# Optimization experiments

Measured on AMD Instinct MI355X. Metric: run time of the kernel, lower is better.

The kernel has to match this reference:

```python
import jax, jax.numpy as jnp
import numpy as np

B, N, F, H, M, EF, OUT = 256, 32, 40, 100, 100, 4, 128
MESSAGE_PASSES = 3


def setup_inputs() -> dict:
    key = jax.random.key(0)
    ks = jax.random.split(key, 8)
    # Deterministic ring graphs: node i <-> node (i+1)%N, one-hot bond type.
    # Every node has degree 2 -> static nonzero counts.
    rng = np.random.default_rng(0)
    edges = np.zeros((B, N, N, EF), np.float32)
    b = np.arange(B)[:, None]
    i = np.arange(N)[None, :]
    j = (i + 1) % N
    t = rng.integers(0, EF, size=(B, N))
    edges[b, i, j, t] = 1.0
    edges[b, j, i, t] = 1.0

    nodes = jax.random.normal(ks[0], (B, N, F), jnp.float32)

    def init(k, shape, fan):
        return jax.random.normal(k, shape, jnp.float32) / np.sqrt(fan).astype(np.float32)

    W_msg = init(ks[1], (M, H, EF), H)          # MNN edge-conditioned weights
    W_ih = init(ks[2], (3 * H, M), M)            # GRUCell input weights
    W_hh = init(ks[3], (3 * H, H), H)            # GRUCell hidden weights
    b_ih = jnp.zeros((3 * H,), jnp.float32)
    b_hh = jnp.zeros((3 * H,), jnp.float32)
    Wg = init(ks[4], (H + F, H), H + F)          # gather gate
    bg = jnp.zeros((H,), jnp.float32)
    We = init(ks[5], (H, H), H)                  # gather embed
    be = jnp.zeros((H,), jnp.float32)
    Wo = init(ks[6], (H, OUT), H)                # output head
    bo = jnp.zeros((OUT,), jnp.float32)

    return {
        "nodes": nodes, "edges": jnp.asarray(edges),
        "W_msg": W_msg, "W_ih": W_ih, "W_hh": W_hh, "b_ih": b_ih, "b_hh": b_hh,
        "Wg": Wg, "bg": bg, "We": We, "be": be, "Wo": Wo, "bo": bo,
        "n_edges": B * N * 2, "n_node_entries": B * N,
    }


def gru_cell(x, h, W_ih, W_hh, b_ih, b_hh):
    gi = x @ W_ih.T + b_ih
    gh = h @ W_hh.T + b_hh
    ir, iz, inn = jnp.split(gi, 3, axis=-1)
    hr, hz, hn = jnp.split(gh, 3, axis=-1)
    r = jax.nn.sigmoid(ir + hr)
    z = jax.nn.sigmoid(iz + hz)
    n = jnp.tanh(inn + r * hn)
    return (1.0 - z) * n + z * h


def reference(nodes, edges, W_msg, W_ih, W_hh, b_ih, b_hh, Wg, bg, We, be, Wo, bo,
              n_edges, n_node_entries):
    adjacency = jnp.sum(edges, axis=3)                      # (B, N, N)
    eb, en, eg = jnp.nonzero(adjacency, size=n_edges)       # edge-level indices
    nb, nn_ = jnp.nonzero(adjacency.sum(-1), size=n_node_entries)

    # Dense one-hot segment-sum matrix: (n_node_entries, n_edges)
    same = (nb[:, None] == eb) & (nn_[:, None] == en)
    msg_sum_mat = same.astype(jnp.float32)

    edge_batch_edges = edges[eb, en, eg, :]                 # (E, EF)

    hidden = jnp.zeros((B, N, H), jnp.float32).at[:, :, :F].set(nodes)
    node_h = hidden[nb, nn_, :]                             # (V, H)

    for _ in range(MESSAGE_PASSES):
        nghb_h = hidden[eb, eg, :]                          # (E, H)
        # MNN message: sum_f edges[e,f] * W_msg[m,h,f] * nghb[e,h]
        message_terms = jnp.einsum('ef,mhf,eh->em', edge_batch_edges, W_msg, nghb_h)
        messages = msg_sum_mat @ message_terms              # (V, M) dense one-hot matmul
        node_h = gru_cell(messages, node_h, W_ih, W_hh, b_ih, b_hh)
        hidden = hidden.at[nb, nn_, :].set(node_h)

    node_mask = (adjacency.sum(-1) != 0).astype(jnp.float32)  # (B, N)
    cat = jnp.concatenate([hidden, nodes], axis=-1)           # (B, N, H+F)
    gate = jax.nn.sigmoid(cat @ Wg + bg)
    emb = gate * (hidden @ We + be)
    graph_emb = jnp.sum(emb * node_mask[..., None], axis=1)   # (B, H)
    return graph_emb @ Wo + bo                                # (B, OUT)
```

## Files before the change

### kernel.cpp

```cpp
#include <hip/hip_runtime.h>
#include <cstddef>
#include <cstdint>

#define B_   256
#define N_   32
#define F_   40
#define H_   100
#define OUT_ 128
#define TB   1024
#define XCS  168
#define XMS  136
#define ST2  40
#define NBLK 343
#define NLO  63

using bf16x8 = __attribute__((ext_vector_type(8))) short;
using f32x4  = __attribute__((ext_vector_type(4))) float;

#define MFMA(a,b,c) __builtin_amdgcn_mfma_f32_16x16x32_bf16((a),(b),(c),0,0,0)

__device__ __forceinline__ float sigmoidf_(float x){ return 1.0f/(1.0f+__expf(-x)); }
__device__ __forceinline__ float tanhf_(float x){
  float e = __expf(2.0f*x);
  return 1.0f - 2.0f/(e+1.0f);
}
__device__ __forceinline__ float bf2f(short s){ return __uint_as_float(((uint32_t)(uint16_t)s)<<16); }
__device__ __forceinline__ short f2bf(float x){
  uint32_t u = __float_as_uint(x);
  return (short)((u + 0x7FFFu + ((u>>16)&1u))>>16);
}
__device__ __forceinline__ void bsplit(float x, short& hi, short& lo){
  hi = f2bf(x);
  lo = f2bf(x - bf2f(hi));
}

__global__ void prep_frags4(const float* __restrict__ Wmsg,
                            const float* __restrict__ Wih,
                            const float* __restrict__ Whh,
                            const float* __restrict__ Wg,
                            const float* __restrict__ We,
                            short* __restrict__ AFhi,
                            short* __restrict__ AFlo){
  int slot = blockIdx.x*blockDim.x + threadIdx.x;
  if (slot >= NBLK*512) return;
  int blk = slot>>9, r = slot&511, lane = r>>3, jj = r&7;
  int m = lane&15, q = lane>>4, kl = q*8+jj;
  float v = 0.0f;
  if (blk < 112){
    int t = blk/28, rem = blk%28, jmt = rem>>2, ks = rem&3;
    int mg = jmt*16+m, h = ks*32+kl;
    if (mg<100 && h<100) v = Wmsg[(mg*100+h)*4 + t];
    AFhi[slot] = f2bf(v);
  } else if (blk < 280){
    int bb = blk-112, mat = bb/28, rem = bb%28, jmt = rem>>2, ks = rem&3;
    int mg = jmt*16+m, k = ks*32+kl;
    if (mg<100 && k<100)
      v = (mat<3) ? Wih[(mat*100+mg)*100+k] : Whh[((mat-3)*100+mg)*100+k];
    AFhi[slot] = f2bf(v);
  } else if (blk < 315){
    int bb = blk-280, jmt = bb/5, ks = bb%5;
    int mg = jmt*16+m, k = ks*32+kl;
    if (mg<100 && k<140) v = Wg[k*100+mg];
    short hi,lo; bsplit(v,hi,lo);
    AFhi[slot] = hi;
    AFlo[(size_t)(blk-280)*512 + r] = lo;
  } else {
    int bb = blk-315, jmt = bb>>2, ks = bb&3;
    int mg = jmt*16+m, k = ks*32+kl;
    if (mg<100 && k<100) v = We[k*100+mg];
    short hi,lo; bsplit(v,hi,lo);
    AFhi[slot] = hi;
    AFlo[(size_t)(blk-280)*512 + r] = lo;
  }
}

__global__ __launch_bounds__(TB, 4) void mpnn_mfma(
    const float* __restrict__ nodes, const float* __restrict__ edges,
    const short* __restrict__ AFhi, const short* __restrict__ AFlo,
    const float* __restrict__ b_ih, const float* __restrict__ b_hh,
    const float* __restrict__ bg, const float* __restrict__ be,
    const float* __restrict__ Wo, const float* __restrict__ bo,
    float* __restrict__ out){
  const int b = blockIdx.x;
  const int tid = threadIdx.x;
  const int lane = tid & 63;
  const int w = tid >> 6;

  __shared__ short XcH[32*XCS];
  __shared__ short XcT[112*ST2];
  __shared__ short XmH[32*XMS];
  __shared__ short XyH[4][32*XMS];
  __shared__ short Aw[4][32*32];
  __shared__ float sh_ge[H_];
  __shared__ float sh_part[4][OUT_];
  __shared__ float sh_rowsum[N_];

  for (int i=tid;i<(32*XCS)/2;i+=TB){ ((int*)XcH)[i]=0; }
  for (int i=tid;i<(32*XMS)/2;i+=TB){ ((int*)XmH)[i]=0; }
  for (int i=tid;i<(112*ST2)/2;i+=TB){ ((int*)XcT)[i]=0; }
  for (int i=tid;i<(4*32*XMS)/2;i+=TB){ ((int*)XyH)[i]=0; }
  if (tid < H_) sh_ge[tid]=0.0f;
  if (tid < N_) sh_rowsum[tid]=0.0f;
  __syncthreads();

  {
    int n = tid>>5, g = tid&31;
    const float4 ev = *(const float4*)(edges + (((size_t)b*N_+n)*N_+g)*4);
    float adj = ev.x+ev.y+ev.z+ev.w;
    if (adj != 0.0f) atomicAdd(&sh_rowsum[n], adj);
    Aw[0][n*32+g] = f2bf(ev.x);
    Aw[1][n*32+g] = f2bf(ev.y);
    Aw[2][n*32+g] = f2bf(ev.z);
    Aw[3][n*32+g] = f2bf(ev.w);
  }
  for (int p=tid; p<N_*F_; p+=TB){
    int n = p/F_, f = p%F_;
    float x = nodes[((size_t)b*N_+n)*F_ + f];
    short hi = f2bf(x);
    XcH[n*XCS+f]=hi;
    XcH[n*XCS+100+f]=hi;
    XcT[f*ST2+n]=hi;
  }

  const int jmt = w>>1, nt = w&1;
  const bool task = (w < 14);
  const int nrow = nt*16 + (lane&15);
  const int boff = (lane>>4)*8;
  const int rowbase = jmt*16 + (lane>>4)*4;

  float hst[4] = {0.f,0.f,0.f,0.f};
  if (task){
#pragma unroll
    for (int r=0;r<4;++r){
      int row = rowbase + r;
      if (row < F_) hst[r] = nodes[((size_t)b*N_+nrow)*F_ + row];
    }
  }
  __syncthreads();

  for (int pass=0; pass<3; ++pass){
    f32x4 Ch0=(f32x4)0.0f, Ch1=(f32x4)0.0f, Ch2=(f32x4)0.0f;
    if (task){
      {
        bf16x8 at = *(const bf16x8*)&XcT[(jmt*16+(lane&15))*ST2 + boff];
        int kbase = jmt*16 + (boff>>1);
#pragma unroll
        for (int t=0;t<4;++t){
          bf16x8 bt = *(const bf16x8*)&Aw[t][nrow*32 + boff];
          f32x4 D = (f32x4)0.0f;
          D = MFMA(at, bt, D);
          short4 pk;
          pk.x = f2bf(D[0]); pk.y = f2bf(D[1]);
          pk.z = f2bf(D[2]); pk.w = f2bf(D[3]);
          *(short4*)&XyH[t][nrow*XMS + kbase] = pk;
        }
      }
      {
        const short* pb = XcH + nrow*XCS + boff;
        bf16x8 b0 = *(const bf16x8*)(pb);
        bf16x8 b1 = *(const bf16x8*)(pb+32);
        bf16x8 b2 = *(const bf16x8*)(pb+64);
        bf16x8 b3 = *(const bf16x8*)(pb+96);
        const short* pa = AFhi + ((size_t)(112 + 3*28 + jmt*4))*512 + lane*8;
        {
          bf16x8 a0=*(const bf16x8*)(pa),      a1=*(const bf16x8*)(pa+512);
          bf16x8 a2=*(const bf16x8*)(pa+1024), a3=*(const bf16x8*)(pa+1536);
          Ch0 = MFMA(a0,b0,Ch0); Ch0 = MFMA(a1,b1,Ch0);
          Ch0 = MFMA(a2,b2,Ch0); Ch0 = MFMA(a3,b3,Ch0);
        }
        pa += 28*512;
        {
          bf16x8 a0=*(const bf16x8*)(pa),      a1=*(const bf16x8*)(pa+512);
          bf16x8 a2=*(const bf16x8*)(pa+1024), a3=*(const bf16x8*)(pa+1536);
          Ch1 = MFMA(a0,b0,Ch1); Ch1 = MFMA(a1,b1,Ch1);
          Ch1 = MFMA(a2,b2,Ch1); Ch1 = MFMA(a3,b3,Ch1);
        }
        pa += 28*512;
        {
          bf16x8 a0=*(const bf16x8*)(pa),      a1=*(const bf16x8*)(pa+512);
          bf16x8 a2=*(const bf16x8*)(pa+1024), a3=*(const bf16x8*)(pa+1536);
          Ch2 = MFMA(a0,b0,Ch2); Ch2 = MFMA(a1,b1,Ch2);
          Ch2 = MFMA(a2,b2,Ch2); Ch2 = MFMA(a3,b3,Ch2);
        }
      }
    }
    __syncthreads();
    if (task){
      f32x4 Cm=(f32x4)0.0f;
#pragma unroll 1
      for (int t=0;t<4;++t){
        const short* pa = AFhi + ((size_t)(t*28 + jmt*4))*512 + lane*8;
        const short* pb = XyH[t] + nrow*XMS + boff;
        bf16x8 a0 = *(const bf16x8*)(pa);
        bf16x8 a1 = *(const bf16x8*)(pa+512);
        bf16x8 a2 = *(const bf16x8*)(pa+1024);
        bf16x8 a3 = *(const bf16x8*)(pa+1536);
        bf16x8 b0 = *(const bf16x8*)(pb);
        bf16x8 b1 = *(const bf16x8*)(pb+32);
        bf16x8 b2 = *(const bf16x8*)(pb+64);
        bf16x8 b3 = *(const bf16x8*)(pb+96);
        Cm = MFMA(a0,b0,Cm); Cm = MFMA(a1,b1,Cm);
        Cm = MFMA(a2,b2,Cm); Cm = MFMA(a3,b3,Cm);
      }
      if (rowbase < 100){
        short4 pk;
        pk.x = f2bf(Cm[0]); pk.y = f2bf(Cm[1]);
        pk.z = f2bf(Cm[2]); pk.w = f2bf(Cm[3]);
        *(short4*)&XmH[nrow*XMS + rowbase] = pk;
      }
    }
    __syncthreads();
    if (task){
      f32x4 Ci0=(f32x4)0.0f, Ci1=(f32x4)0.0f, Ci2=(f32x4)0.0f;
      {
        const short* pb = XmH + nrow*XMS + boff;
        bf16x8 b0 = *(const bf16x8*)(pb);
        bf16x8 b1 = *(const bf16x8*)(pb+32);
        bf16x8 b2 = *(const bf16x8*)(pb+64);
        bf16x8 b3 = *(const bf16x8*)(pb+96);
        const short* pa = AFhi + ((size_t)(112 + jmt*4))*512 + lane*8;
        {
          bf16x8 a0=*(const bf16x8*)(pa),      a1=*(const bf16x8*)(pa+512);
          bf16x8 a2=*(const bf16x8*)(pa+1024), a3=*(const bf16x8*)(pa+1536);
          Ci0 = MFMA(a0,b0,Ci0); Ci0 = MFMA(a1,b1,Ci0);
          Ci0 = MFMA(a2,b2,Ci0); Ci0 = MFMA(a3,b3,Ci0);
        }
        pa += 28*512;
        {
          bf16x8 a0=*(const bf16x8*)(pa),      a1=*(const bf16x8*)(pa+512);
          bf16x8 a2=*(const bf16x8*)(pa+1024), a3=*(const bf16x8*)(pa+1536);
          Ci1 = MFMA(a0,b0,Ci1); Ci1 = MFMA(a1,b1,Ci1);
          Ci1 = MFMA(a2,b2,Ci1); Ci1 = MFMA(a3,b3,Ci1);
        }
        pa += 28*512;
        {
          bf16x8 a0=*(const bf16x8*)(pa),      a1=*(const bf16x8*)(pa+512);
          bf16x8 a2=*(const bf16x8*)(pa+1024), a3=*(const bf16x8*)(pa+1536);
          Ci2 = MFMA(a0,b0,Ci2); Ci2 = MFMA(a1,b1,Ci2);
          Ci2 = MFMA(a2,b2,Ci2); Ci2 = MFMA(a3,b3,Ci2);
        }
      }
      if (rowbase < 100){
        bool msk = (sh_rowsum[nrow] != 0.0f);
        short4 pk;
#pragma unroll
        for (int r=0;r<4;++r){
          int row = rowbase + r;
          float ho = hst[r];
          float rr = sigmoidf_(Ci0[r]+Ch0[r] + b_ih[row]     + b_hh[row]);
          float zz = sigmoidf_(Ci1[r]+Ch1[r] + b_ih[100+row] + b_hh[100+row]);
          float nn = tanhf_(Ci2[r] + b_ih[200+row] + rr*(Ch2[r] + b_hh[200+row]));
          float hnew = (1.0f-zz)*nn + zz*ho;
          if (!msk) hnew = ho;
          hst[r] = hnew;
          short hb = f2bf(hnew);
          ((short*)&pk)[r] = hb;
          XcT[row*ST2+nrow] = hb;
        }
        *(short4*)&XcH[nrow*XCS + rowbase] = pk;
      }
    }
    __syncthreads();
  }

  f32x4 Cg=(f32x4)0.0f, Ce=(f32x4)0.0f;
  if (task){
    const short* pb = XcH + nrow*XCS + boff;
    bf16x8 b0 = *(const bf16x8*)(pb);
    bf16x8 b1 = *(const bf16x8*)(pb+32);
    bf16x8 b2 = *(const bf16x8*)(pb+64);
    bf16x8 b3 = *(const bf16x8*)(pb+96);
    bf16x8 b4 = *(const bf16x8*)(pb+128);
    {
      const short* ph = AFhi + ((size_t)(280 + jmt*5))*512 + lane*8;
      const short* pl = AFlo + ((size_t)(jmt*5))*512 + lane*8;
      Cg = MFMA(*(const bf16x8*)(ph),      b0, Cg);
      Cg = MFMA(*(const bf16x8*)(pl),      b0, Cg);
      Cg = MFMA(*(const bf16x8*)(ph+512),  b1, Cg);
      Cg = MFMA(*(const bf16x8*)(pl+512),  b1, Cg);
      Cg = MFMA(*(const bf16x8*)(ph+1024), b2, Cg);
      Cg = MFMA(*(const bf16x8*)(pl+1024), b2, Cg);
      Cg = MFMA(*(const bf16x8*)(ph+1536), b3, Cg);
      Cg = MFMA(*(const bf16x8*)(pl+1536), b3, Cg);
      Cg = MFMA(*(const bf16x8*)(ph+2048), b4, Cg);
      Cg = MFMA(*(const bf16x8*)(pl+2048), b4, Cg);
    }
    {
      const short* ph = AFhi + ((size_t)(315 + jmt*4))*512 + lane*8;
      const short* pl = AFlo + ((size_t)(35 + jmt*4))*512 + lane*8;
      Ce = MFMA(*(const bf16x8*)(ph),      b0, Ce);
      Ce = MFMA(*(const bf16x8*)(pl),      b0, Ce);
      Ce = MFMA(*(const bf16x8*)(ph+512),  b1, Ce);
      Ce = MFMA(*(const bf16x8*)(pl+512),  b1, Ce);
      Ce = MFMA(*(const bf16x8*)(ph+1024), b2, Ce);
      Ce = MFMA(*(const bf16x8*)(pl+1024), b2, Ce);
      Ce = MFMA(*(const bf16x8*)(ph+1536), b3, Ce);
      Ce = MFMA(*(const bf16x8*)(pl+1536), b3, Ce);
    }
    bool msk = (sh_rowsum[nrow] != 0.0f);
#pragma unroll
    for (int r=0;r<4;++r){
      int row = rowbase + r;
      float v = 0.0f;
      if (row<100){
        float gate = sigmoidf_(Cg[r] + bg[row]);
        float emb  = gate*(Ce[r] + be[row]);
        v = msk ? emb : 0.0f;
      }
      v += __shfl_xor(v, 1);
      v += __shfl_xor(v, 2);
      v += __shfl_xor(v, 4);
      v += __shfl_xor(v, 8);
      if (row<100 && (lane&15)==0) atomicAdd(&sh_ge[row], v);
    }
  }
  __syncthreads();
  if (tid < 512){
    int o = tid & 127, q = tid >> 7;
    float s = 0.0f;
    int k0 = 25*q;
#pragma unroll 5
    for (int k=k0; k<k0+25; ++k) s += sh_ge[k]*Wo[k*OUT_+o];
    sh_part[q][o] = s;
  }
  __syncthreads();
  if (tid < OUT_){
    out[(size_t)b*OUT_ + tid] = bo[tid] + sh_part[0][tid] + sh_part[1][tid]
                              + sh_part[2][tid] + sh_part[3][tid];
  }
}

extern "C" void kernel_launch(void* const* d_in, const int* in_sizes, int n_in,
                              void* d_out, int out_size, void* d_ws, size_t ws_size,
                              hipStream_t stream){
  const float* nodes = (const float*)d_in[0];
  const float* edges = (const float*)d_in[1];
  const float* W_msg = (const float*)d_in[2];
  const float* W_ih  = (const float*)d_in[3];
  const float* W_hh  = (const float*)d_in[4];
  const float* b_ih  = (const float*)d_in[5];
  const float* b_hh  = (const float*)d_in[6];
  const float* Wg    = (const float*)d_in[7];
  const float* bg    = (const float*)d_in[8];
  const float* We    = (const float*)d_in[9];
  const float* be    = (const float*)d_in[10];
  const float* Wo    = (const float*)d_in[11];
  const float* bo    = (const float*)d_in[12];

  short* AFhi = (short*)d_ws;
  short* AFlo = AFhi + (size_t)NBLK*512;

  prep_frags4<<<(NBLK*512 + 255)/256, 256, 0, stream>>>(W_msg, W_ih, W_hh, Wg, We,
                                                        AFhi, AFlo);
  mpnn_mfma<<<B_, TB, 0, stream>>>(nodes, edges, AFhi, AFlo, b_ih, b_hh, bg, be,
                                   Wo, bo, (float*)d_out);
}
```

Measured before the change: 113.3 us.

## Fold W_msg into W_ih to drop the message stage and one barrier

Precomputes fused weights W_ih·W_msg[:,:,t] for each gate and edge type in the prep kernel, so each pass goes straight from the per-type neighbour aggregates to the GRU input gates. This removes the intermediate message buffer, its bf16 rounding, and one block-wide barrier per pass, but triples the A-fragment loads in that stage (12 MFMA groups instead of 4+3). The row-mask is also computed with a wavefront ballot instead of shared atomics. The prep kernel now runs a 100-term dot product per element, which adds prep cost and changes rounding.

Result: slower. 137.4 us (+21.3%).

```diff
diff --git a/kernel.cpp b/kernel.cpp
--- a/kernel.cpp
+++ b/kernel.cpp
@@ -11,7 +11,7 @@
 #define XCS  168
 #define XMS  136
 #define ST2  40
-#define NBLK 343
+#define NBLK 483
 #define NLO  63
 
 using bf16x8 = __attribute__((ext_vector_type(8))) short;
@@ -34,7 +34,7 @@
   lo = f2bf(x - bf2f(hi));
 }
 
-__global__ void prep_frags4(const float* __restrict__ Wmsg,
+__global__ void prep_frags5(const float* __restrict__ Wmsg,
                             const float* __restrict__ Wih,
                             const float* __restrict__ Whh,
                             const float* __restrict__ Wg,
@@ -46,31 +46,38 @@
   int blk = slot>>9, r = slot&511, lane = r>>3, jj = r&7;
   int m = lane&15, q = lane>>4, kl = q*8+jj;
   float v = 0.0f;
-  if (blk < 112){
-    int t = blk/28, rem = blk%28, jmt = rem>>2, ks = rem&3;
-    int mg = jmt*16+m, h = ks*32+kl;
-    if (mg<100 && h<100) v = Wmsg[(mg*100+h)*4 + t];
+  if (blk < 336){
+    int mt = blk/28, rem = blk%28, jmt = rem>>2, ks = rem&3;
+    int mat = mt>>2, t = mt&3;
+    int rr = jmt*16+m, h = ks*32+kl;
+    if (rr<100 && h<100){
+      const float* wih = Wih + ((size_t)(mat*100+rr))*100;
+      const float* wm  = Wmsg + (size_t)h*4 + t;
+      float s = 0.0f;
+#pragma unroll 4
+      for (int mp=0; mp<100; ++mp) s += wih[mp]*wm[(size_t)mp*400];
+      v = s;
+    }
     AFhi[slot] = f2bf(v);
-  } else if (blk < 280){
-    int bb = blk-112, mat = bb/28, rem = bb%28, jmt = rem>>2, ks = rem&3;
+  } else if (blk < 420){
+    int bb = blk-336, mat = bb/28, rem = bb%28, jmt = rem>>2, ks = rem&3;
     int mg = jmt*16+m, k = ks*32+kl;
-    if (mg<100 && k<100)
-      v = (mat<3) ? Wih[(mat*100+mg)*100+k] : Whh[((mat-3)*100+mg)*100+k];
+    if (mg<100 && k<100) v = Whh[((size_t)(mat*100+mg))*100+k];
     AFhi[slot] = f2bf(v);
-  } else if (blk < 315){
-    int bb = blk-280, jmt = bb/5, ks = bb%5;
+  } else if (blk < 455){
+    int bb = blk-420, jmt = bb/5, ks = bb%5;
     int mg = jmt*16+m, k = ks*32+kl;
-    if (mg<100 && k<140) v = Wg[k*100+mg];
+    if (mg<100 && k<140) v = Wg[(size_t)k*100+mg];
     short hi,lo; bsplit(v,hi,lo);
     AFhi[slot] = hi;
-    AFlo[(size_t)(blk-280)*512 + r] = lo;
+    AFlo[(size_t)(blk-420)*512 + r] = lo;
   } else {
-    int bb = blk-315, jmt = bb>>2, ks = bb&3;
+    int bb = blk-455, jmt = bb>>2, ks = bb&3;
     int mg = jmt*16+m, k = ks*32+kl;
-    if (mg<100 && k<100) v = We[k*100+mg];
+    if (mg<100 && k<100) v = We[(size_t)k*100+mg];
     short hi,lo; bsplit(v,hi,lo);
     AFhi[slot] = hi;
-    AFlo[(size_t)(blk-280)*512 + r] = lo;
+    AFlo[(size_t)(blk-420)*512 + r] = lo;
   }
 }
 
@@ -88,26 +95,25 @@
 
   __shared__ short XcH[32*XCS];
   __shared__ short XcT[112*ST2];
-  __shared__ short XmH[32*XMS];
   __shared__ short XyH[4][32*XMS];
   __shared__ short Aw[4][32*32];
   __shared__ float sh_ge[H_];
   __shared__ float sh_part[4][OUT_];
-  __shared__ float sh_rowsum[N_];
+  __shared__ int   sh_msk[N_];
 
   for (int i=tid;i<(32*XCS)/2;i+=TB){ ((int*)XcH)[i]=0; }
-  for (int i=tid;i<(32*XMS)/2;i+=TB){ ((int*)XmH)[i]=0; }
   for (int i=tid;i<(112*ST2)/2;i+=TB){ ((int*)XcT)[i]=0; }
   for (int i=tid;i<(4*32*XMS)/2;i+=TB){ ((int*)XyH)[i]=0; }
   if (tid < H_) sh_ge[tid]=0.0f;
-  if (tid < N_) sh_rowsum[tid]=0.0f;
   __syncthreads();
 
   {
     int n = tid>>5, g = tid&31;
     const float4 ev = *(const float4*)(edges + (((size_t)b*N_+n)*N_+g)*4);
     float adj = ev.x+ev.y+ev.z+ev.w;
-    if (adj != 0.0f) atomicAdd(&sh_rowsum[n], adj);
+    unsigned long long bal = __ballot(adj != 0.0f);
+    if (lane == 0)  sh_msk[n] = ((int)(bal & 0xFFFFFFFFull)) != 0;
+    if (lane == 32) sh_msk[n] = ((int)(bal >> 32)) != 0;
     Aw[0][n*32+g] = f2bf(ev.x);
     Aw[1][n*32+g] = f2bf(ev.y);
     Aw[2][n*32+g] = f2bf(ev.z);
@@ -161,7 +167,7 @@
         bf16x8 b1 = *(const bf16x8*)(pb+32);
         bf16x8 b2 = *(const bf16x8*)(pb+64);
         bf16x8 b3 = *(const bf16x8*)(pb+96);
-        const short* pa = AFhi + ((size_t)(112 + 3*28 + jmt*4))*512 + lane*8;
+        const short* pa = AFhi + ((size_t)(336 + jmt*4))*512 + lane*8;
         {
           bf16x8 a0=*(const bf16x8*)(pa),      a1=*(const bf16x8*)(pa+512);
           bf16x8 a2=*(const bf16x8*)(pa+1024), a3=*(const bf16x8*)(pa+1536);
@@ -186,53 +192,29 @@
     }
     __syncthreads();
     if (task){
-      f32x4 Cm=(f32x4)0.0f;
+      f32x4 Ci0=(f32x4)0.0f, Ci1=(f32x4)0.0f, Ci2=(f32x4)0.0f;
 #pragma unroll 1
       for (int t=0;t<4;++t){
-        const short* pa = AFhi + ((size_t)(t*28 + jmt*4))*512 + lane*8;
         const short* pb = XyH[t] + nrow*XMS + boff;
-        bf16x8 a0 = *(const bf16x8*)(pa);
-        bf16x8 a1 = *(const bf16x8*)(pa+512);
-        bf16x8 a2 = *(const bf16x8*)(pa+1024);
-        bf16x8 a3 = *(const bf16x8*)(pa+1536);
         bf16x8 b0 = *(const bf16x8*)(pb);
         bf16x8 b1 = *(const bf16x8*)(pb+32);
         bf16x8 b2 = *(const bf16x8*)(pb+64);
         bf16x8 b3 = *(const bf16x8*)(pb+96);
-        Cm = MFMA(a0,b0,Cm); Cm = MFMA(a1,b1,Cm);
-        Cm = MFMA(a2,b2,Cm); Cm = MFMA(a3,b3,Cm);
-      }
-      if (rowbase < 100){
-        short4 pk;
-        pk.x = f2bf(Cm[0]); pk.y = f2bf(Cm[1]);
-        pk.z = f2bf(Cm[2]); pk.w = f2bf(Cm[3]);
-        *(short4*)&XmH[nrow*XMS + rowbase] = pk;
-      }
-    }
-    __syncthreads();
-    if (task){
-      f32x4 Ci0=(f32x4)0.0f, Ci1=(f32x4)0.0f, Ci2=(f32x4)0.0f;
-      {
-        const short* pb = XmH + nrow*XMS + boff;
-        bf16x8 b0 = *(const bf16x8*)(pb);
-        bf16x8 b1 = *(const bf16x8*)(pb+32);
-        bf16x8 b2 = *(const bf16x8*)(pb+64);
-        bf16x8 b3 = *(const bf16x8*)(pb+96);
-        const short* pa = AFhi + ((size_t)(112 + jmt*4))*512 + lane*8;
+        const short* pa = AFhi + ((size_t)(t*28 + jmt*4))*512 + lane*8;
         {
           bf16x8 a0=*(const bf16x8*)(pa),      a1=*(const bf16x8*)(pa+512);
           bf16x8 a2=*(const bf16x8*)(pa+1024), a3=*(const bf16x8*)(pa+1536);
           Ci0 = MFMA(a0,b0,Ci0); Ci0 = MFMA(a1,b1,Ci0);
           Ci0 = MFMA(a2,b2,Ci0); Ci0 = MFMA(a3,b3,Ci0);
         }
-        pa += 28*512;
+        pa += 112*512;
         {
           bf16x8 a0=*(const bf16x8*)(pa),      a1=*(const bf16x8*)(pa+512);
           bf16x8 a2=*(const bf16x8*)(pa+1024), a3=*(const bf16x8*)(pa+1536);
           Ci1 = MFMA(a0,b0,Ci1); Ci1 = MFMA(a1,b1,Ci1);
           Ci1 = MFMA(a2,b2,Ci1); Ci1 = MFMA(a3,b3,Ci1);
         }
-        pa += 28*512;
+        pa += 112*512;
         {
           bf16x8 a0=*(const bf16x8*)(pa),      a1=*(const bf16x8*)(pa+512);
           bf16x8 a2=*(const bf16x8*)(pa+1024), a3=*(const bf16x8*)(pa+1536);
@@ -241,7 +223,7 @@
         }
       }
       if (rowbase < 100){
-        bool msk = (sh_rowsum[nrow] != 0.0f);
+        bool msk = sh_msk[nrow] != 0;
         short4 pk;
 #pragma unroll
         for (int r=0;r<4;++r){
@@ -272,7 +254,7 @@
     bf16x8 b3 = *(const bf16x8*)(pb+96);
     bf16x8 b4 = *(const bf16x8*)(pb+128);
     {
-      const short* ph = AFhi + ((size_t)(280 + jmt*5))*512 + lane*8;
+      const short* ph = AFhi + ((size_t)(420 + jmt*5))*512 + lane*8;
       const short* pl = AFlo + ((size_t)(jmt*5))*512 + lane*8;
       Cg = MFMA(*(const bf16x8*)(ph),      b0, Cg);
       Cg = MFMA(*(const bf16x8*)(pl),      b0, Cg);
@@ -286,7 +268,7 @@
       Cg = MFMA(*(const bf16x8*)(pl+2048), b4, Cg);
     }
     {
-      const short* ph = AFhi + ((size_t)(315 + jmt*4))*512 + lane*8;
+      const short* ph = AFhi + ((size_t)(455 + jmt*4))*512 + lane*8;
       const short* pl = AFlo + ((size_t)(35 + jmt*4))*512 + lane*8;
       Ce = MFMA(*(const bf16x8*)(ph),      b0, Ce);
       Ce = MFMA(*(const bf16x8*)(pl),      b0, Ce);
@@ -297,7 +279,7 @@
       Ce = MFMA(*(const bf16x8*)(ph+1536), b3, Ce);
       Ce = MFMA(*(const bf16x8*)(pl+1536), b3, Ce);
     }
-    bool msk = (sh_rowsum[nrow] != 0.0f);
+    bool msk = sh_msk[nrow] != 0;
 #pragma unroll
     for (int r=0;r<4;++r){
       int row = rowbase + r;
@@ -350,7 +332,7 @@
   short* AFhi = (short*)d_ws;
   short* AFlo = AFhi + (size_t)NBLK*512;
 
-  prep_frags4<<<(NBLK*512 + 255)/256, 256, 0, stream>>>(W_msg, W_ih, W_hh, Wg, We,
+  prep_frags5<<<(NBLK*512 + 255)/256, 256, 0, stream>>>(W_msg, W_ih, W_hh, Wg, We,
                                                         AFhi, AFlo);
   mpnn_mfma<<<B_, TB, 0, stream>>>(nodes, edges, AFhi, AFlo, b_ih, b_hh, bg, be,
                                    Wo, bo, (float*)d_out);
```

## Reassociate message matmul to apply W_msg before adjacency and drop a barrier

Applied to the files above, without the earlier changes.

Changes the message computation from (adjacency x hidden) then W_msg to (W_msg x hidden) then adjacency, per edge type. Each warp computes its own Z tile in a private LDS scratch area, which removes the transposed hidden copy, the XyH buffers and one block-wide barrier per pass. The cost is more MFMA work per warp (two 4-step chains per edge type instead of one MFMA), and the bf16 rounding now happens at a different intermediate. The row mask is also computed with a wave ballot instead of LDS atomics.

New measurement: 123.0 us. 1.09x slower.

```diff
diff --git a/kernel.cpp b/kernel.cpp
--- a/kernel.cpp
+++ b/kernel.cpp
@@ -10,7 +10,8 @@
 #define TB   1024
 #define XCS  168
 #define XMS  136
-#define ST2  40
+#define AWS  40
+#define ZSP  40
 #define NBLK 343
 #define NLO  63
 
@@ -87,31 +88,29 @@
   const int w = tid >> 6;
 
   __shared__ short XcH[32*XCS];
-  __shared__ short XcT[112*ST2];
   __shared__ short XmH[32*XMS];
-  __shared__ short XyH[4][32*XMS];
-  __shared__ short Aw[4][32*32];
+  __shared__ short Aw[4][32*AWS];
+  __shared__ short Zs[14*16*ZSP];
   __shared__ float sh_ge[H_];
   __shared__ float sh_part[4][OUT_];
-  __shared__ float sh_rowsum[N_];
+  __shared__ int   sh_msk[N_];
 
   for (int i=tid;i<(32*XCS)/2;i+=TB){ ((int*)XcH)[i]=0; }
   for (int i=tid;i<(32*XMS)/2;i+=TB){ ((int*)XmH)[i]=0; }
-  for (int i=tid;i<(112*ST2)/2;i+=TB){ ((int*)XcT)[i]=0; }
-  for (int i=tid;i<(4*32*XMS)/2;i+=TB){ ((int*)XyH)[i]=0; }
   if (tid < H_) sh_ge[tid]=0.0f;
-  if (tid < N_) sh_rowsum[tid]=0.0f;
   __syncthreads();
 
   {
     int n = tid>>5, g = tid&31;
     const float4 ev = *(const float4*)(edges + (((size_t)b*N_+n)*N_+g)*4);
     float adj = ev.x+ev.y+ev.z+ev.w;
-    if (adj != 0.0f) atomicAdd(&sh_rowsum[n], adj);
-    Aw[0][n*32+g] = f2bf(ev.x);
-    Aw[1][n*32+g] = f2bf(ev.y);
-    Aw[2][n*32+g] = f2bf(ev.z);
-    Aw[3][n*32+g] = f2bf(ev.w);
+    unsigned long long bal = __ballot(adj != 0.0f);
+    if (lane == 0)  sh_msk[n] = ((int)(bal & 0xFFFFFFFFull)) != 0;
+    if (lane == 32) sh_msk[n] = ((int)(bal >> 32)) != 0;
+    Aw[0][n*AWS+g] = f2bf(ev.x);
+    Aw[1][n*AWS+g] = f2bf(ev.y);
+    Aw[2][n*AWS+g] = f2bf(ev.z);
+    Aw[3][n*AWS+g] = f2bf(ev.w);
   }
   for (int p=tid; p<N_*F_; p+=TB){
     int n = p/F_, f = p%F_;
@@ -119,7 +118,6 @@
     short hi = f2bf(x);
     XcH[n*XCS+f]=hi;
     XcH[n*XCS+100+f]=hi;
-    XcT[f*ST2+n]=hi;
   }
 
   const int jmt = w>>1, nt = w&1;
@@ -127,6 +125,9 @@
   const int nrow = nt*16 + (lane&15);
   const int boff = (lane>>4)*8;
   const int rowbase = jmt*16 + (lane>>4)*4;
+  const int zb = w*16*ZSP;
+  const int zcol = lane&15;
+  const int zrow = (lane>>4)*4;
 
   float hst[4] = {0.f,0.f,0.f,0.f};
   if (task){
@@ -141,20 +142,6 @@
   for (int pass=0; pass<3; ++pass){
     f32x4 Ch0=(f32x4)0.0f, Ch1=(f32x4)0.0f, Ch2=(f32x4)0.0f;
     if (task){
-      {
-        bf16x8 at = *(const bf16x8*)&XcT[(jmt*16+(lane&15))*ST2 + boff];
-        int kbase = jmt*16 + (boff>>1);
-#pragma unroll
-        for (int t=0;t<4;++t){
-          bf16x8 bt = *(const bf16x8*)&Aw[t][nrow*32 + boff];
-          f32x4 D = (f32x4)0.0f;
-          D = MFMA(at, bt, D);
-          short4 pk;
-          pk.x = f2bf(D[0]); pk.y = f2bf(D[1]);
-          pk.z = f2bf(D[2]); pk.w = f2bf(D[3]);
-          *(short4*)&XyH[t][nrow*XMS + kbase] = pk;
-        }
-      }
       {
         const short* pb = XcH + nrow*XCS + boff;
         bf16x8 b0 = *(const bf16x8*)(pb);
@@ -183,30 +170,41 @@
           Ch2 = MFMA(a2,b2,Ch2); Ch2 = MFMA(a3,b3,Ch2);
         }
       }
-    }
-    __syncthreads();
-    if (task){
-      f32x4 Cm=(f32x4)0.0f;
+      {
+        f32x4 Cm=(f32x4)0.0f;
 #pragma unroll 1
-      for (int t=0;t<4;++t){
-        const short* pa = AFhi + ((size_t)(t*28 + jmt*4))*512 + lane*8;
-        const short* pb = XyH[t] + nrow*XMS + boff;
-        bf16x8 a0 = *(const bf16x8*)(pa);
-        bf16x8 a1 = *(const bf16x8*)(pa+512);
-        bf16x8 a2 = *(const bf16x8*)(pa+1024);
-        bf16x8 a3 = *(const bf16x8*)(pa+1536);
-        bf16x8 b0 = *(const bf16x8*)(pb);
-        bf16x8 b1 = *(const bf16x8*)(pb+32);
-        bf16x8 b2 = *(const bf16x8*)(pb+64);
-        bf16x8 b3 = *(const bf16x8*)(pb+96);
-        Cm = MFMA(a0,b0,Cm); Cm = MFMA(a1,b1,Cm);
-        Cm = MFMA(a2,b2,Cm); Cm = MFMA(a3,b3,Cm);
-      }
-      if (rowbase < 100){
-        short4 pk;
-        pk.x = f2bf(Cm[0]); pk.y = f2bf(Cm[1]);
-        pk.z = f2bf(Cm[2]); pk.w = f2bf(Cm[3]);
-        *(short4*)&XmH[nrow*XMS + rowbase] = pk;
+        for (int t=0;t<4;++t){
+          const short* pa = AFhi + ((size_t)(t*28 + jmt*4))*512 + lane*8;
+          bf16x8 a0 = *(const bf16x8*)(pa);
+          bf16x8 a1 = *(const bf16x8*)(pa+512);
+          bf16x8 a2 = *(const bf16x8*)(pa+1024);
+          bf16x8 a3 = *(const bf16x8*)(pa+1536);
+          const short* pg0 = XcH + (lane&15)*XCS + boff;
+          const short* pg1 = pg0 + 16*XCS;
+          f32x4 Z0=(f32x4)0.0f, Z1=(f32x4)0.0f;
+          Z0 = MFMA(a0, *(const bf16x8*)(pg0),    Z0);
+          Z0 = MFMA(a1, *(const bf16x8*)(pg0+32), Z0);
+          Z0 = MFMA(a2, *(const bf16x8*)(pg0+64), Z0);
+          Z0 = MFMA(a3, *(const bf16x8*)(pg0+96), Z0);
+          Z1 = MFMA(a0, *(const bf16x8*)(pg1),    Z1);
+          Z1 = MFMA(a1, *(const bf16x8*)(pg1+32), Z1);
+          Z1 = MFMA(a2, *(const bf16x8*)(pg1+64), Z1);
+          Z1 = MFMA(a3, *(const bf16x8*)(pg1+96), Z1);
+#pragma unroll
+          for (int r=0;r<4;++r){
+            Zs[zb + (zrow+r)*ZSP + zcol]      = f2bf(Z0[r]);
+            Zs[zb + (zrow+r)*ZSP + zcol + 16] = f2bf(Z1[r]);
+          }
+          bf16x8 az = *(const bf16x8*)&Zs[zb + (lane&15)*ZSP + boff];
+          bf16x8 bt = *(const bf16x8*)&Aw[t][nrow*AWS + boff];
+          Cm = MFMA(az, bt, Cm);
+        }
+        if (rowbase < 100){
+          short4 pk;
+          pk.x = f2bf(Cm[0]); pk.y = f2bf(Cm[1]);
+          pk.z = f2bf(Cm[2]); pk.w = f2bf(Cm[3]);
+          *(short4*)&XmH[nrow*XMS + rowbase] = pk;
+        }
       }
     }
     __syncthreads();
@@ -241,7 +239,7 @@
         }
       }
       if (rowbase < 100){
-        bool msk = (sh_rowsum[nrow] != 0.0f);
+        bool msk = sh_msk[nrow] != 0;
         short4 pk;
 #pragma unroll
         for (int r=0;r<4;++r){
@@ -253,9 +251,7 @@
           float hnew = (1.0f-zz)*nn + zz*ho;
           if (!msk) hnew = ho;
           hst[r] = hnew;
-          short hb = f2bf(hnew);
-          ((short*)&pk)[r] = hb;
-          XcT[row*ST2+nrow] = hb;
+          ((short*)&pk)[r] = f2bf(hnew);
         }
         *(short4*)&XcH[nrow*XCS + rowbase] = pk;
       }
@@ -297,7 +293,7 @@
       Ce = MFMA(*(const bf16x8*)(ph+1536), b3, Ce);
       Ce = MFMA(*(const bf16x8*)(pl+1536), b3, Ce);
     }
-    bool msk = (sh_rowsum[nrow] != 0.0f);
+    bool msk = sh_msk[nrow] != 0;
 #pragma unroll
     for (int r=0;r<4;++r){
       int row = rowbase + r;
```
